# Kernel tuning notes

Measured on AMD Instinct MI355X. Metric: run time of the kernel, lower is better.

Reference implementation:

```python
import jax, jax.numpy as jnp
import numpy as np

B, S, D, H = 2, 2048, 1024, 16
DH = D // H


def setup_inputs() -> dict:
    key = jax.random.key(0)
    ks = jax.random.split(key, 5)
    scale = 0.02
    return {
        "X": jax.random.normal(ks[0], (B, S, D), jnp.float32),
        "Wq": jax.random.normal(ks[1], (H, D, DH), jnp.float32) * scale,
        "Wk": jax.random.normal(ks[2], (H, D, DH), jnp.float32) * scale,
        "Wv": jax.random.normal(ks[3], (H, D, DH), jnp.float32) * scale,
        "Wo": jax.random.normal(ks[4], (D, D), jnp.float32) * scale,
        "bo": jnp.zeros((D,), jnp.float32),
    }


def reference(X, Wq, Wk, Wv, Wo, bo):
    # Per-head projections, batched over heads: [B,H,S,DH]
    Q = jnp.einsum('bsd,hde->bhse', X, Wq)
    K = jnp.einsum('bsd,hde->bhse', X, Wk)
    V = jnp.einsum('bsd,hde->bhse', X, Wv)
    # Scores scaled by sqrt(d_model) exactly as in the source (not sqrt(d_head))
    A = jnp.einsum('bhse,bhte->bhst', Q, K) / jnp.sqrt(jnp.float32(D))
    A = jax.nn.softmax(A, axis=-1)  # no mask in the source
    O = jnp.einsum('bhst,bhte->bhse', A, V)  # [B,H,S,DH]
    # Concat heads -> [B,S,D], then output projection
    O = jnp.transpose(O, (0, 2, 1, 3)).reshape(B, S, D)
    return O @ Wo + bo
```

## Files before the change

kernel.cpp:

```cpp
#include <hip/hip_runtime.h>
#include <math.h>

static constexpr int Bc  = 2;
static constexpr int Sc  = 2048;
static constexpr int Dc  = 1024;
static constexpr int Hc  = 16;
static constexpr int DHc = 64;

typedef short bf16x8 __attribute__((ext_vector_type(8)));
typedef float f32x4  __attribute__((ext_vector_type(4)));

static __device__ __forceinline__ unsigned short f2bf(float x) {
  union { float f; unsigned u; } v; v.f = x;
  unsigned r = v.u + 0x7FFFu + ((v.u >> 16) & 1u);
  return (unsigned short)(r >> 16);
}
static __device__ __forceinline__ float bf2f(unsigned short u) {
  union { unsigned u; float f; } v; v.u = ((unsigned)u) << 16;
  return v.f;
}

static __device__ __forceinline__ void gload16(const void* g, void* l) {
  __builtin_amdgcn_global_load_lds(
      (const __attribute__((address_space(1))) void*)g,
      (__attribute__((address_space(3))) void*)l, 16, 0, 0);
}

__global__ __launch_bounds__(256) void convert_x(
    const float* __restrict__ X, unsigned short* __restrict__ Xb) {
  int i = blockIdx.x * 256 + threadIdx.x;
  float4 v = ((const float4*)X)[i];
  ushort4 u; u.x = f2bf(v.x); u.y = f2bf(v.y); u.z = f2bf(v.z); u.w = f2bf(v.w);
  ((ushort4*)Xb)[i] = u;
}

__global__ __launch_bounds__(256) void transpose_w(
    const float* __restrict__ Wq, const float* __restrict__ Wk,
    const float* __restrict__ Wv, const float* __restrict__ Wo,
    unsigned short* __restrict__ Wt3, unsigned short* __restrict__ Wot) {
  __shared__ unsigned short T[64][68];
  const int z = blockIdx.z;
  const float* src; unsigned short* dst;
  int srcld, dstld, r0, c0;
  if (z < 3) {
    const float* W = (z == 0) ? Wq : (z == 1) ? Wk : Wv;
    unsigned short* Wt = Wt3 + (size_t)z * Dc * Dc;
    int h = blockIdx.y;
    src = W + (size_t)h * Dc * DHc;  srcld = DHc; r0 = blockIdx.x * 64; c0 = 0;
    dst = Wt + (size_t)h * DHc * Dc; dstld = Dc;
  } else {
    src = Wo;  srcld = Dc; r0 = blockIdx.x * 64; c0 = blockIdx.y * 64;
    dst = Wot; dstld = Dc;
  }
#pragma unroll
  for (int it = 0; it < 16; ++it) {
    int idx = it * 256 + threadIdx.x;
    int r = idx >> 6, c = idx & 63;
    T[c][r] = f2bf(src[(size_t)(r0 + r) * srcld + c0 + c]);
  }
  __syncthreads();
#pragma unroll
  for (int it = 0; it < 4; ++it) {
    int idx = it * 256 + threadIdx.x;
    int c = idx >> 4, r4 = (idx & 15) * 4;
    ushort4 u = *(const ushort4*)&T[c][r4];
    *(ushort4*)&dst[(size_t)(c0 + c) * dstld + r0 + r4] = u;
  }
}

__global__ __launch_bounds__(256) void qkv_gemm(
    const unsigned short* __restrict__ Xb, const unsigned short* __restrict__ Wt3,
    unsigned short* __restrict__ Qb, unsigned short* __restrict__ Kb,
    unsigned short* __restrict__ Vtb) {
  __shared__ alignas(16) unsigned char smem[35072];
  unsigned short (*As)[64] = (unsigned short(*)[64])smem;
  unsigned short (*Bs)[64] = (unsigned short(*)[64])(smem + 16384);

  const int tid = threadIdx.x;
  const int wv = tid >> 6, lane = tid & 63;
  const int ln = tid & 15, qd = (tid >> 4) & 3;
  const int wm = wv >> 1, wn = wv & 1;
  const int m0 = blockIdx.x * 128;
  const int y  = blockIdx.y;
  const int n0 = y * 128;
  const int which = y >> 3;
  const int lr = lane >> 3, lc = (lane & 7) * 8;

  f32x4 acc[4][4];
#pragma unroll
  for (int mt = 0; mt < 4; ++mt)
#pragma unroll
    for (int nt = 0; nt < 4; ++nt) acc[mt][nt] = (f32x4){0.f, 0.f, 0.f, 0.f};

  for (int k0 = 0; k0 < Dc; k0 += 64) {
    __syncthreads();
#pragma unroll
    for (int t = 0; t < 4; ++t) {
      gload16(Xb  + (size_t)(m0 + wv * 32 + t * 8 + lr) * Dc + k0 + lc, &As[wv * 32 + t * 8][0]);
      gload16(Wt3 + (size_t)(n0 + wv * 32 + t * 8 + lr) * Dc + k0 + lc, &Bs[wv * 32 + t * 8][0]);
    }
    __syncthreads();
#pragma unroll
    for (int ks = 0; ks < 2; ++ks) {
      bf16x8 af[4], bf[4];
#pragma unroll
      for (int mt = 0; mt < 4; ++mt)
        af[mt] = *(const bf16x8*)&As[wm * 64 + mt * 16 + ln][ks * 32 + qd * 8];
#pragma unroll
      for (int nt = 0; nt < 4; ++nt)
        bf[nt] = *(const bf16x8*)&Bs[wn * 64 + nt * 16 + ln][ks * 32 + qd * 8];
#pragma unroll
      for (int mt = 0; mt < 4; ++mt)
#pragma unroll
        for (int nt = 0; nt < 4; ++nt)
          acc[mt][nt] = __builtin_amdgcn_mfma_f32_16x16x32_bf16(af[mt], bf[nt], acc[mt][nt], 0, 0, 0);
    }
  }

  const int b = m0 >> 11, s0 = m0 & 2047;

  if (which < 2) {
    unsigned short* Out = (which == 0) ? Qb : Kb;
    const float scale = (which == 0) ? (1.0f / 32.0f) : 1.0f;
#pragma unroll
    for (int mt = 0; mt < 4; ++mt)
#pragma unroll
      for (int r = 0; r < 4; ++r) {
        int s = s0 + wm * 64 + mt * 16 + qd * 4 + r;
#pragma unroll
        for (int nt = 0; nt < 4; ++nt) {
          int n = (n0 & 1023) + wn * 64 + nt * 16 + ln;
          int h = n >> 6, e = n & 63;
          Out[(((size_t)b * Hc + h) * Sc + s) * DHc + e] = f2bf(acc[mt][nt][r] * scale);
        }
      }
  } else {
    __syncthreads();
    unsigned short* Ts = (unsigned short*)smem;
    const int hb = (y & 7) * 2;
#pragma unroll
    for (int mt = 0; mt < 4; ++mt)
#pragma unroll
      for (int r = 0; r < 4; ++r)
#pragma unroll
        for (int nt = 0; nt < 4; ++nt)
          Ts[(wm * 64 + mt * 16 + qd * 4 + r) * 137 + wn * 64 + nt * 16 + ln] =
              f2bf(acc[mt][nt][r]);
    __syncthreads();
#pragma unroll
    for (int hh = 0; hh < 2; ++hh) {
      int bh = b * Hc + hb + hh;
#pragma unroll
      for (int it = 0; it < 8; ++it) {
        int idx = it * 256 + tid;
        int e = idx >> 5, s4 = (idx & 31) * 4;
        ushort4 u;
        u.x = Ts[(s4 + 0) * 137 + hh * 64 + e];
        u.y = Ts[(s4 + 1) * 137 + hh * 64 + e];
        u.z = Ts[(s4 + 2) * 137 + hh * 64 + e];
        u.w = Ts[(s4 + 3) * 137 + hh * 64 + e];
        *(ushort4*)&Vtb[((size_t)bh * DHc + e) * Sc + s0 + s4] = u;
      }
    }
  }
}

__global__ __launch_bounds__(256) void attn_partial(
    const unsigned short* __restrict__ Qb, const unsigned short* __restrict__ Kb,
    const unsigned short* __restrict__ Vtb,
    unsigned short* __restrict__ Opart, float* __restrict__ lpart) {
  __shared__ alignas(16) unsigned short Ks[64][64];
  __shared__ alignas(16) unsigned short Vts[64][64];
  __shared__ alignas(16) unsigned short Ps[128][72];

  const int tid = threadIdx.x;
  const int wv = tid >> 6, lane = tid & 63;
  const int ln = tid & 15, qd = (tid >> 4) & 3;
  const int sT = blockIdx.x, bh = blockIdx.y, sp = blockIdx.z;
  const int lr = lane >> 3, lc = (lane & 7) * 8;

  bf16x8 qf[2][2];
  const size_t qrow0 = (size_t)bh * Sc + sT * 128 + wv * 32;
#pragma unroll
  for (int mt = 0; mt < 2; ++mt)
#pragma unroll
    for (int ks = 0; ks < 2; ++ks)
      qf[mt][ks] = *(const bf16x8*)&Qb[(qrow0 + mt * 16 + ln) * DHc + ks * 32 + qd * 8];

  f32x4 o[2][4];
#pragma unroll
  for (int mt = 0; mt < 2; ++mt)
#pragma unroll
    for (int et = 0; et < 4; ++et) o[mt][et] = (f32x4){0.f, 0.f, 0.f, 0.f};
  float lsum[2] = {0.f, 0.f};

  for (int kb = sp * 16; kb < sp * 16 + 16; ++kb) {
    __syncthreads();
#pragma unroll
    for (int t = 0; t < 2; ++t) {
      gload16(Kb  + ((size_t)bh * Sc + kb * 64 + wv * 16 + t * 8 + lr) * DHc + lc,
              &Ks[wv * 16 + t * 8][0]);
      gload16(Vtb + ((size_t)bh * DHc + wv * 16 + t * 8 + lr) * Sc + kb * 64 + lc,
              &Vts[wv * 16 + t * 8][0]);
    }
    __syncthreads();

    f32x4 st[2][4];
#pragma unroll
    for (int mt = 0; mt < 2; ++mt)
#pragma unroll
      for (int nt = 0; nt < 4; ++nt) st[mt][nt] = (f32x4){0.f, 0.f, 0.f, 0.f};
#pragma unroll
    for (int ks = 0; ks < 2; ++ks) {
#pragma unroll
      for (int nt = 0; nt < 4; ++nt) {
        bf16x8 kf = *(const bf16x8*)&Ks[nt * 16 + ln][ks * 32 + qd * 8];
#pragma unroll
        for (int mt = 0; mt < 2; ++mt)
          st[mt][nt] = __builtin_amdgcn_mfma_f32_16x16x32_bf16(kf, qf[mt][ks], st[mt][nt], 0, 0, 0);
      }
    }

#pragma unroll
    for (int mt = 0; mt < 2; ++mt)
#pragma unroll
      for (int nt = 0; nt < 4; ++nt) {
        float p0 = __expf(st[mt][nt][0]);
        float p1 = __expf(st[mt][nt][1]);
        float p2 = __expf(st[mt][nt][2]);
        float p3 = __expf(st[mt][nt][3]);
        lsum[mt] += (p0 + p1) + (p2 + p3);
        ushort4 u; u.x = f2bf(p0); u.y = f2bf(p1); u.z = f2bf(p2); u.w = f2bf(p3);
        *(ushort4*)&Ps[wv * 32 + mt * 16 + ln][nt * 16 + qd * 4] = u;
      }
    __syncthreads();

#pragma unroll
    for (int ks = 0; ks < 2; ++ks) {
      bf16x8 pf[2];
#pragma unroll
      for (int mt = 0; mt < 2; ++mt)
        pf[mt] = *(const bf16x8*)&Ps[wv * 32 + mt * 16 + ln][ks * 32 + qd * 8];
#pragma unroll
      for (int et = 0; et < 4; ++et) {
        bf16x8 vf = *(const bf16x8*)&Vts[et * 16 + ln][ks * 32 + qd * 8];
#pragma unroll
        for (int mt = 0; mt < 2; ++mt)
          o[mt][et] = __builtin_amdgcn_mfma_f32_16x16x32_bf16(pf[mt], vf, o[mt][et], 0, 0, 0);
      }
    }
  }

  const size_t pbase = ((size_t)sp * 512 + bh * 16 + sT) * 128;
#pragma unroll
  for (int mt = 0; mt < 2; ++mt) {
    float ls = lsum[mt];
    ls += __shfl_xor(ls, 16);
    ls += __shfl_xor(ls, 32);
    if (qd == 0) lpart[pbase + wv * 32 + mt * 16 + ln] = ls;
  }
#pragma unroll
  for (int mt = 0; mt < 2; ++mt)
#pragma unroll
    for (int r = 0; r < 4; ++r) {
      int row = wv * 32 + mt * 16 + qd * 4 + r;
#pragma unroll
      for (int et = 0; et < 4; ++et)
        Opart[(pbase + row) * DHc + et * 16 + ln] = f2bf(o[mt][et][r]);
    }
}

__global__ __launch_bounds__(256) void combine(
    const unsigned short* __restrict__ Opart, const float* __restrict__ lpart,
    unsigned short* __restrict__ Ocat) {
  const int sT = blockIdx.x, bh = blockIdx.y, tid = threadIdx.x;
  const int b = bh >> 4, h = bh & 15;
  const size_t p0 = ((size_t)bh * 16 + sT) * 128;
  const size_t p1 = ((size_t)512 + bh * 16 + sT) * 128;
#pragma unroll
  for (int it = 0; it < 8; ++it) {
    int idx = it * 256 + tid;
    int row = idx >> 4, c4 = (idx & 15) * 4;
    ushort4 u0 = *(const ushort4*)&Opart[(p0 + row) * DHc + c4];
    ushort4 u1 = *(const ushort4*)&Opart[(p1 + row) * DHc + c4];
    float inv = 1.0f / (lpart[p0 + row] + lpart[p1 + row]);
    ushort4 w;
    w.x = f2bf((bf2f(u0.x) + bf2f(u1.x)) * inv);
    w.y = f2bf((bf2f(u0.y) + bf2f(u1.y)) * inv);
    w.z = f2bf((bf2f(u0.z) + bf2f(u1.z)) * inv);
    w.w = f2bf((bf2f(u0.w) + bf2f(u1.w)) * inv);
    *(ushort4*)&Ocat[((size_t)b * Sc + sT * 128 + row) * Dc + h * DHc + c4] = w;
  }
}

__global__ __launch_bounds__(256) void out_gemm(
    const unsigned short* __restrict__ Ab, const unsigned short* __restrict__ Wot,
    const float* __restrict__ bo, float* __restrict__ Out) {
  __shared__ alignas(16) unsigned short As[64][64];
  __shared__ alignas(16) unsigned short Bs[128][64];

  const int tid = threadIdx.x;
  const int wv = tid >> 6, lane = tid & 63;
  const int ln = tid & 15, qd = (tid >> 4) & 3;
  const int wm = wv >> 1, wn = wv & 1;
  const int m0 = blockIdx.x * 64, n0 = blockIdx.y * 128;
  const int lr = lane >> 3, lc = (lane & 7) * 8;

  f32x4 acc[2][4];
#pragma unroll
  for (int mt = 0; mt < 2; ++mt)
#pragma unroll
    for (int nt = 0; nt < 4; ++nt) acc[mt][nt] = (f32x4){0.f, 0.f, 0.f, 0.f};

  for (int k0 = 0; k0 < Dc; k0 += 64) {
    __syncthreads();
#pragma unroll
    for (int t = 0; t < 2; ++t)
      gload16(Ab + (size_t)(m0 + wv * 16 + t * 8 + lr) * Dc + k0 + lc, &As[wv * 16 + t * 8][0]);
#pragma unroll
    for (int t = 0; t < 4; ++t)
      gload16(Wot + (size_t)(n0 + wv * 32 + t * 8 + lr) * Dc + k0 + lc, &Bs[wv * 32 + t * 8][0]);
    __syncthreads();
#pragma unroll
    for (int ks = 0; ks < 2; ++ks) {
      bf16x8 af[2], bf[4];
#pragma unroll
      for (int mt = 0; mt < 2; ++mt)
        af[mt] = *(const bf16x8*)&As[wm * 32 + mt * 16 + ln][ks * 32 + qd * 8];
#pragma unroll
      for (int nt = 0; nt < 4; ++nt)
        bf[nt] = *(const bf16x8*)&Bs[wn * 64 + nt * 16 + ln][ks * 32 + qd * 8];
#pragma unroll
      for (int mt = 0; mt < 2; ++mt)
#pragma unroll
        for (int nt = 0; nt < 4; ++nt)
          acc[mt][nt] = __builtin_amdgcn_mfma_f32_16x16x32_bf16(af[mt], bf[nt], acc[mt][nt], 0, 0, 0);
    }
  }

  float bias[4];
#pragma unroll
  for (int nt = 0; nt < 4; ++nt) bias[nt] = bo[n0 + wn * 64 + nt * 16 + ln];

#pragma unroll
  for (int mt = 0; mt < 2; ++mt)
#pragma unroll
    for (int r = 0; r < 4; ++r) {
      int m = m0 + wm * 32 + mt * 16 + qd * 4 + r;
#pragma unroll
      for (int nt = 0; nt < 4; ++nt)
        Out[(size_t)m * Dc + n0 + wn * 64 + nt * 16 + ln] = acc[mt][nt][r] + bias[nt];
    }
}

extern "C" void kernel_launch(void* const* d_in, const int* in_sizes, int n_in,
                              void* d_out, int out_size, void* d_ws, size_t ws_size,
                              hipStream_t stream) {
  (void)in_sizes; (void)n_in; (void)out_size; (void)ws_size;
  const float* X  = (const float*)d_in[0];
  const float* Wq = (const float*)d_in[1];
  const float* Wk = (const float*)d_in[2];
  const float* Wv = (const float*)d_in[3];
  const float* Wo = (const float*)d_in[4];
  const float* bo = (const float*)d_in[5];
  float* out = (float*)d_out;

  const size_t nX = (size_t)Bc * Sc * Dc;
  unsigned short* Xb   = (unsigned short*)d_ws;
  unsigned short* Wt3  = Xb + nX;
  unsigned short* Wot  = Wt3 + (size_t)3 * Dc * Dc;
  unsigned short* Qb   = Wot + (size_t)Dc * Dc;
  unsigned short* Kb   = Qb + nX;
  unsigned short* Vtb  = Kb + nX;
  unsigned short* Opart = Vtb + nX;
  float* lpart = (float*)(Opart + 2 * nX);
  unsigned short* Ocat = Xb;

  convert_x<<<dim3(nX / 1024), 256, 0, stream>>>(X, Xb);
  transpose_w<<<dim3(16, 16, 4), 256, 0, stream>>>(Wq, Wk, Wv, Wo, Wt3, Wot);
  qkv_gemm<<<dim3(32, 24), 256, 0, stream>>>(Xb, Wt3, Qb, Kb, Vtb);
  attn_partial<<<dim3(16, 32, 2), 256, 0, stream>>>(Qb, Kb, Vtb, Opart, lpart);
  combine<<<dim3(16, 32), 256, 0, stream>>>(Opart, lpart, Ocat);
  out_gemm<<<dim3(64, 8), 256, 0, stream>>>(Ocat, Wot, bo, out);
}
```

Before: 214.7 us.

## Swizzle LDS tiles, use exp2 softmax, MFMA row sums, merge prep kernels

Applies an XOR swizzle to the LDS tile layouts in all three GEMM-style kernels to remove bank conflicts, and drops the padding on the P buffer. In the attention kernel, log2(e) is folded into the Q scale so the softmax can use a native exp2. P is packed to bf16 by truncation, and the row sums come from an MFMA against a ones vector instead of shuffles. The X conversion and the weight transpose are merged into one launch. Truncated bf16 P and bf16-summed row sums slightly change numerics.

```diff
diff --git a/kernel.cpp b/kernel.cpp
--- a/kernel.cpp
+++ b/kernel.cpp
@@ -10,6 +10,8 @@
 typedef short bf16x8 __attribute__((ext_vector_type(8)));
 typedef float f32x4  __attribute__((ext_vector_type(4)));
 
+static constexpr float LOG2E = 1.4426950408889634f;
+
 static __device__ __forceinline__ unsigned short f2bf(float x) {
   union { float f; unsigned u; } v; v.f = x;
   unsigned r = v.u + 0x7FFFu + ((v.u >> 16) & 1u);
@@ -19,6 +21,14 @@
   union { unsigned u; float f; } v; v.u = ((unsigned)u) << 16;
   return v.f;
 }
+static __device__ __forceinline__ unsigned pk2bf_trunc(float a, float b) {
+  return __builtin_amdgcn_perm(__float_as_uint(b), __float_as_uint(a), 0x07060302u);
+}
+#if __has_builtin(__builtin_amdgcn_exp2f)
+#define EXP2F(x) __builtin_amdgcn_exp2f(x)
+#else
+#define EXP2F(x) exp2f(x)
+#endif
 
 static __device__ __forceinline__ void gload16(const void* g, void* l) {
   __builtin_amdgcn_global_load_lds(
@@ -26,20 +36,25 @@
       (__attribute__((address_space(3))) void*)l, 16, 0, 0);
 }
 
-__global__ __launch_bounds__(256) void convert_x(
-    const float* __restrict__ X, unsigned short* __restrict__ Xb) {
-  int i = blockIdx.x * 256 + threadIdx.x;
-  float4 v = ((const float4*)X)[i];
-  ushort4 u; u.x = f2bf(v.x); u.y = f2bf(v.y); u.z = f2bf(v.z); u.w = f2bf(v.w);
-  ((ushort4*)Xb)[i] = u;
-}
-
-__global__ __launch_bounds__(256) void transpose_w(
+__global__ __launch_bounds__(256) void prep(
     const float* __restrict__ Wq, const float* __restrict__ Wk,
     const float* __restrict__ Wv, const float* __restrict__ Wo,
-    unsigned short* __restrict__ Wt3, unsigned short* __restrict__ Wot) {
+    const float* __restrict__ X,
+    unsigned short* __restrict__ Wt3, unsigned short* __restrict__ Wot,
+    unsigned short* __restrict__ Xb) {
+  const int z = blockIdx.z;
+  if (z == 4) {
+    size_t base = ((size_t)blockIdx.y * 16 + blockIdx.x) * 4096;
+#pragma unroll
+    for (int it = 0; it < 16; ++it) {
+      size_t i = base + it * 256 + threadIdx.x;
+      float4 v = ((const float4*)X)[i];
+      ushort4 u; u.x = f2bf(v.x); u.y = f2bf(v.y); u.z = f2bf(v.z); u.w = f2bf(v.w);
+      ((ushort4*)Xb)[i] = u;
+    }
+    return;
+  }
   __shared__ unsigned short T[64][68];
-  const int z = blockIdx.z;
   const float* src; unsigned short* dst;
   int srcld, dstld, r0, c0;
   if (z < 3) {
@@ -84,7 +99,8 @@
   const int y  = blockIdx.y;
   const int n0 = y * 128;
   const int which = y >> 3;
-  const int lr = lane >> 3, lc = (lane & 7) * 8;
+  const int lr = lane >> 3;
+  const int lcs = ((lane & 7) ^ lr) * 8;
 
   f32x4 acc[4][4];
 #pragma unroll
@@ -96,19 +112,20 @@
     __syncthreads();
 #pragma unroll
     for (int t = 0; t < 4; ++t) {
-      gload16(Xb  + (size_t)(m0 + wv * 32 + t * 8 + lr) * Dc + k0 + lc, &As[wv * 32 + t * 8][0]);
-      gload16(Wt3 + (size_t)(n0 + wv * 32 + t * 8 + lr) * Dc + k0 + lc, &Bs[wv * 32 + t * 8][0]);
+      gload16(Xb  + (size_t)(m0 + wv * 32 + t * 8 + lr) * Dc + k0 + lcs, &As[wv * 32 + t * 8][0]);
+      gload16(Wt3 + (size_t)(n0 + wv * 32 + t * 8 + lr) * Dc + k0 + lcs, &Bs[wv * 32 + t * 8][0]);
     }
     __syncthreads();
 #pragma unroll
     for (int ks = 0; ks < 2; ++ks) {
+      const int pa = ((ks * 4 + qd) ^ (ln & 7)) * 8;
       bf16x8 af[4], bf[4];
 #pragma unroll
       for (int mt = 0; mt < 4; ++mt)
-        af[mt] = *(const bf16x8*)&As[wm * 64 + mt * 16 + ln][ks * 32 + qd * 8];
+        af[mt] = *(const bf16x8*)&As[wm * 64 + mt * 16 + ln][pa];
 #pragma unroll
       for (int nt = 0; nt < 4; ++nt)
-        bf[nt] = *(const bf16x8*)&Bs[wn * 64 + nt * 16 + ln][ks * 32 + qd * 8];
+        bf[nt] = *(const bf16x8*)&Bs[wn * 64 + nt * 16 + ln][pa];
 #pragma unroll
       for (int mt = 0; mt < 4; ++mt)
 #pragma unroll
@@ -121,7 +138,7 @@
 
   if (which < 2) {
     unsigned short* Out = (which == 0) ? Qb : Kb;
-    const float scale = (which == 0) ? (1.0f / 32.0f) : 1.0f;
+    const float scale = (which == 0) ? (LOG2E / 32.0f) : 1.0f;
 #pragma unroll
     for (int mt = 0; mt < 4; ++mt)
 #pragma unroll
@@ -171,13 +188,14 @@
     unsigned short* __restrict__ Opart, float* __restrict__ lpart) {
   __shared__ alignas(16) unsigned short Ks[64][64];
   __shared__ alignas(16) unsigned short Vts[64][64];
-  __shared__ alignas(16) unsigned short Ps[128][72];
+  __shared__ alignas(16) unsigned short Ps[128][64];
 
   const int tid = threadIdx.x;
   const int wv = tid >> 6, lane = tid & 63;
   const int ln = tid & 15, qd = (tid >> 4) & 3;
   const int sT = blockIdx.x, bh = blockIdx.y, sp = blockIdx.z;
-  const int lr = lane >> 3, lc = (lane & 7) * 8;
+  const int lr = lane >> 3;
+  const int lcs = ((lane & 7) ^ lr) * 8;
 
   bf16x8 qf[2][2];
   const size_t qrow0 = (size_t)bh * Sc + sT * 128 + wv * 32;
@@ -187,20 +205,25 @@
     for (int ks = 0; ks < 2; ++ks)
       qf[mt][ks] = *(const bf16x8*)&Qb[(qrow0 + mt * 16 + ln) * DHc + ks * 32 + qd * 8];
 
-  f32x4 o[2][4];
-#pragma unroll
-  for (int mt = 0; mt < 2; ++mt)
+  bf16x8 vones;
+#pragma unroll
+  for (int j = 0; j < 8; ++j) vones[j] = (short)0x3F80;
+
+  f32x4 o[2][4], lacc[2];
+#pragma unroll
+  for (int mt = 0; mt < 2; ++mt) {
+    lacc[mt] = (f32x4){0.f, 0.f, 0.f, 0.f};
 #pragma unroll
     for (int et = 0; et < 4; ++et) o[mt][et] = (f32x4){0.f, 0.f, 0.f, 0.f};
-  float lsum[2] = {0.f, 0.f};
+  }
 
   for (int kb = sp * 16; kb < sp * 16 + 16; ++kb) {
     __syncthreads();
 #pragma unroll
     for (int t = 0; t < 2; ++t) {
-      gload16(Kb  + ((size_t)bh * Sc + kb * 64 + wv * 16 + t * 8 + lr) * DHc + lc,
+      gload16(Kb  + ((size_t)bh * Sc + kb * 64 + wv * 16 + t * 8 + lr) * DHc + lcs,
               &Ks[wv * 16 + t * 8][0]);
-      gload16(Vtb + ((size_t)bh * DHc + wv * 16 + t * 8 + lr) * Sc + kb * 64 + lc,
+      gload16(Vtb + ((size_t)bh * DHc + wv * 16 + t * 8 + lr) * Sc + kb * 64 + lcs,
               &Vts[wv * 16 + t * 8][0]);
     }
     __syncthreads();
@@ -212,9 +235,10 @@
       for (int nt = 0; nt < 4; ++nt) st[mt][nt] = (f32x4){0.f, 0.f, 0.f, 0.f};
 #pragma unroll
     for (int ks = 0; ks < 2; ++ks) {
+      const int pa = ((ks * 4 + qd) ^ (ln & 7)) * 8;
 #pragma unroll
       for (int nt = 0; nt < 4; ++nt) {
-        bf16x8 kf = *(const bf16x8*)&Ks[nt * 16 + ln][ks * 32 + qd * 8];
+        bf16x8 kf = *(const bf16x8*)&Ks[nt * 16 + ln][pa];
 #pragma unroll
         for (int mt = 0; mt < 2; ++mt)
           st[mt][nt] = __builtin_amdgcn_mfma_f32_16x16x32_bf16(kf, qf[mt][ks], st[mt][nt], 0, 0, 0);
@@ -222,28 +246,35 @@
     }
 
 #pragma unroll
-    for (int mt = 0; mt < 2; ++mt)
+    for (int mt = 0; mt < 2; ++mt) {
+      const int prow = wv * 32 + mt * 16 + ln;
 #pragma unroll
       for (int nt = 0; nt < 4; ++nt) {
-        float p0 = __expf(st[mt][nt][0]);
-        float p1 = __expf(st[mt][nt][1]);
-        float p2 = __expf(st[mt][nt][2]);
-        float p3 = __expf(st[mt][nt][3]);
-        lsum[mt] += (p0 + p1) + (p2 + p3);
-        ushort4 u; u.x = f2bf(p0); u.y = f2bf(p1); u.z = f2bf(p2); u.w = f2bf(p3);
-        *(ushort4*)&Ps[wv * 32 + mt * 16 + ln][nt * 16 + qd * 4] = u;
-      }
+        float p0 = EXP2F(st[mt][nt][0]);
+        float p1 = EXP2F(st[mt][nt][1]);
+        float p2 = EXP2F(st[mt][nt][2]);
+        float p3 = EXP2F(st[mt][nt][3]);
+        uint2 w;
+        w.x = pk2bf_trunc(p0, p1);
+        w.y = pk2bf_trunc(p2, p3);
+        int ppos = ((2 * nt + (qd >> 1)) ^ (ln & 7)) * 8 + (qd & 1) * 4;
+        *(uint2*)&Ps[prow][ppos] = w;
+      }
+    }
     __syncthreads();
 
 #pragma unroll
     for (int ks = 0; ks < 2; ++ks) {
+      const int pa = ((ks * 4 + qd) ^ (ln & 7)) * 8;
       bf16x8 pf[2];
 #pragma unroll
-      for (int mt = 0; mt < 2; ++mt)
-        pf[mt] = *(const bf16x8*)&Ps[wv * 32 + mt * 16 + ln][ks * 32 + qd * 8];
+      for (int mt = 0; mt < 2; ++mt) {
+        pf[mt] = *(const bf16x8*)&Ps[wv * 32 + mt * 16 + ln][pa];
+        lacc[mt] = __builtin_amdgcn_mfma_f32_16x16x32_bf16(pf[mt], vones, lacc[mt], 0, 0, 0);
+      }
 #pragma unroll
       for (int et = 0; et < 4; ++et) {
-        bf16x8 vf = *(const bf16x8*)&Vts[et * 16 + ln][ks * 32 + qd * 8];
+        bf16x8 vf = *(const bf16x8*)&Vts[et * 16 + ln][pa];
 #pragma unroll
         for (int mt = 0; mt < 2; ++mt)
           o[mt][et] = __builtin_amdgcn_mfma_f32_16x16x32_bf16(pf[mt], vf, o[mt][et], 0, 0, 0);
@@ -252,12 +283,12 @@
   }
 
   const size_t pbase = ((size_t)sp * 512 + bh * 16 + sT) * 128;
-#pragma unroll
-  for (int mt = 0; mt < 2; ++mt) {
-    float ls = lsum[mt];
-    ls += __shfl_xor(ls, 16);
-    ls += __shfl_xor(ls, 32);
-    if (qd == 0) lpart[pbase + wv * 32 + mt * 16 + ln] = ls;
+  if (ln == 0) {
+#pragma unroll
+    for (int mt = 0; mt < 2; ++mt)
+#pragma unroll
+      for (int r = 0; r < 4; ++r)
+        lpart[pbase + wv * 32 + mt * 16 + qd * 4 + r] = lacc[mt][r];
   }
 #pragma unroll
   for (int mt = 0; mt < 2; ++mt)
@@ -304,7 +335,8 @@
   const int ln = tid & 15, qd = (tid >> 4) & 3;
   const int wm = wv >> 1, wn = wv & 1;
   const int m0 = blockIdx.x * 64, n0 = blockIdx.y * 128;
-  const int lr = lane >> 3, lc = (lane & 7) * 8;
+  const int lr = lane >> 3;
+  const int lcs = ((lane & 7) ^ lr) * 8;
 
   f32x4 acc[2][4];
 #pragma unroll
@@ -316,20 +348,21 @@
     __syncthreads();
 #pragma unroll
     for (int t = 0; t < 2; ++t)
-      gload16(Ab + (size_t)(m0 + wv * 16 + t * 8 + lr) * Dc + k0 + lc, &As[wv * 16 + t * 8][0]);
+      gload16(Ab + (size_t)(m0 + wv * 16 + t * 8 + lr) * Dc + k0 + lcs, &As[wv * 16 + t * 8][0]);
 #pragma unroll
     for (int t = 0; t < 4; ++t)
-      gload16(Wot + (size_t)(n0 + wv * 32 + t * 8 + lr) * Dc + k0 + lc, &Bs[wv * 32 + t * 8][0]);
+      gload16(Wot + (size_t)(n0 + wv * 32 + t * 8 + lr) * Dc + k0 + lcs, &Bs[wv * 32 + t * 8][0]);
     __syncthreads();
 #pragma unroll
     for (int ks = 0; ks < 2; ++ks) {
+      const int pa = ((ks * 4 + qd) ^ (ln & 7)) * 8;
       bf16x8 af[2], bf[4];
 #pragma unroll
       for (int mt = 0; mt < 2; ++mt)
-        af[mt] = *(const bf16x8*)&As[wm * 32 + mt * 16 + ln][ks * 32 + qd * 8];
+        af[mt] = *(const bf16x8*)&As[wm * 32 + mt * 16 + ln][pa];
 #pragma unroll
       for (int nt = 0; nt < 4; ++nt)
-        bf[nt] = *(const bf16x8*)&Bs[wn * 64 + nt * 16 + ln][ks * 32 + qd * 8];
+        bf[nt] = *(const bf16x8*)&Bs[wn * 64 + nt * 16 + ln][pa];
 #pragma unroll
       for (int mt = 0; mt < 2; ++mt)
 #pragma unroll
@@ -366,18 +399,17 @@
   float* out = (float*)d_out;
 
   const size_t nX = (size_t)Bc * Sc * Dc;
-  unsigned short* Xb   = (unsigned short*)d_ws;
-  unsigned short* Wt3  = Xb + nX;
-  unsigned short* Wot  = Wt3 + (size_t)3 * Dc * Dc;
-  unsigned short* Qb   = Wot + (size_t)Dc * Dc;
-  unsigned short* Kb   = Qb + nX;
-  unsigned short* Vtb  = Kb + nX;
+  unsigned short* Xb    = (unsigned short*)d_ws;
+  unsigned short* Wt3   = Xb + nX;
+  unsigned short* Wot   = Wt3 + (size_t)3 * Dc * Dc;
+  unsigned short* Qb    = Wot + (size_t)Dc * Dc;
+  unsigned short* Kb    = Qb + nX;
+  unsigned short* Vtb   = Kb + nX;
   unsigned short* Opart = Vtb + nX;
   float* lpart = (float*)(Opart + 2 * nX);
   unsigned short* Ocat = Xb;
 
-  convert_x<<<dim3(nX / 1024), 256, 0, stream>>>(X, Xb);
-  transpose_w<<<dim3(16, 16, 4), 256, 0, stream>>>(Wq, Wk, Wv, Wo, Wt3, Wot);
+  prep<<<dim3(16, 16, 5), 256, 0, stream>>>(Wq, Wk, Wv, Wo, X, Wt3, Wot, Xb);
   qkv_gemm<<<dim3(32, 24), 256, 0, stream>>>(Xb, Wt3, Qb, Kb, Vtb);
   attn_partial<<<dim3(16, 32, 2), 256, 0, stream>>>(Qb, Kb, Vtb, Opart, lpart);
   combine<<<dim3(16, 32), 256, 0, stream>>>(Opart, lpart, Ocat);
```

Measured after the change: 199.4 us. -7.1%, faster.
